# Optimization experiments

Hardware: AMD Instinct MI355X
Metric: run time of the kernel (lower is better)

## Reference

```python
import jax, jax.numpy as jnp
import numpy as np

B, S, D = 2, 2048, 4096
H, KV, HD = 32, 8, 128
THETA = 10000.0


def rotate_half(x):
    x1, x2 = x[..., : HD // 2], x[..., HD // 2 :]
    return jnp.concatenate((-x2, x1), axis=-1)


def setup_inputs() -> dict:
    key = jax.random.key(0)
    ks = jax.random.split(key, 8)
    s = 1.0 / np.sqrt(D)
    return {
        "hidden_states": jax.random.normal(ks[0], (B, S, D), jnp.float32),
        "modality_indicators": jax.random.randint(ks[1], (B, S), 0, 2, jnp.int64 if jax.config.jax_enable_x64 else jnp.int32),
        "position_ids": jnp.arange(S, dtype=jnp.int32),
        "Wq": jax.random.normal(ks[2], (D, H * HD), jnp.float32) * s,
        "Wk0": jax.random.normal(ks[3], (D, KV * HD), jnp.float32) * s,
        "Wk1": jax.random.normal(ks[4], (D, KV * HD), jnp.float32) * s,
        "Wv0": jax.random.normal(ks[5], (D, KV * HD), jnp.float32) * s,
        "Wv1": jax.random.normal(ks[6], (D, KV * HD), jnp.float32) * s,
        "Wo": jax.random.normal(ks[7], (H * HD, D), jnp.float32) * s,
    }


def reference(hidden_states, modality_indicators, position_ids, Wq, Wk0, Wk1, Wv0, Wv1, Wo):
    x = hidden_states
    # Multiway (modality-routed) k/v projections: per-token select between two linears.
    sel = (modality_indicators == 1)[..., None]  # [B,S,1]
    q = x @ Wq                                   # [B,S,H*HD]
    k = jnp.where(sel, x @ Wk1, x @ Wk0)         # [B,S,KV*HD]
    v = jnp.where(sel, x @ Wv1, x @ Wv0)

    q = q.reshape(B, S, H, HD).transpose(0, 2, 1, 3)    # [B,H,S,HD]
    k = k.reshape(B, S, KV, HD).transpose(0, 2, 1, 3)   # [B,KV,S,HD]
    v = v.reshape(B, S, KV, HD).transpose(0, 2, 1, 3)

    # RoPE cache and application (emb = cat(freqs, freqs))
    inv_freq = 1.0 / (THETA ** (jnp.arange(0, HD, 2, dtype=jnp.float32) / HD))
    freqs = position_ids.astype(jnp.float32)[:, None] * inv_freq[None, :]   # [S,HD/2]
    emb = jnp.concatenate((freqs, freqs), axis=-1)                          # [S,HD]
    cos = jnp.cos(emb)[None, None, :, :]                                    # [1,1,S,HD]
    sin = jnp.sin(emb)[None, None, :, :]
    q = q * cos + rotate_half(q) * sin
    k = k * cos + rotate_half(k) * sin

    # GQA: repeat kv heads
    n_rep = H // KV
    k = jnp.repeat(k, n_rep, axis=1)  # [B,H,S,HD]
    v = jnp.repeat(v, n_rep, axis=1)

    scores = jnp.einsum("bhqd,bhkd->bhqk", q, k) / np.sqrt(HD)
    causal = jnp.tril(jnp.ones((S, S), dtype=bool))
    scores = jnp.where(causal[None, None], scores, jnp.finfo(scores.dtype).min)
    attn = jax.nn.softmax(scores, axis=-1)
    ctx = jnp.einsum("bhqk,bhkd->bhqd", attn, v)            # [B,H,S,HD]
    ctx = ctx.transpose(0, 2, 1, 3).reshape(B, S, H * HD)
    return ctx @ Wo
```

## Files before the change

### kernel.cpp

```cpp
#include <hip/hip_runtime.h>

typedef unsigned short u16;
typedef unsigned int   u32;
using bf16x8 = __attribute__((ext_vector_type(8))) __bf16;
using f32x4  = __attribute__((ext_vector_type(4))) float;
using f32x16 = __attribute__((ext_vector_type(16))) float;
using u32x4  = __attribute__((ext_vector_type(4))) unsigned int;


__device__ __forceinline__ u16 f2bf(float f) {
  u32 u = __builtin_bit_cast(u32, f);
  return (u16)((u + 0x7fffu + ((u >> 16) & 1u)) >> 16);
}
__device__ __forceinline__ float bf2f(u16 h) {
  return __builtin_bit_cast(float, (u32)h << 16);
}
__device__ __forceinline__ f32x4 mfma16(bf16x8 a, bf16x8 b, f32x4 c) {
  return __builtin_amdgcn_mfma_f32_16x16x32_bf16(a, b, c, 0, 0, 0);
}
__device__ __forceinline__ f32x16 mfma32(bf16x8 a, bf16x8 b, f32x16 c) {
  return __builtin_amdgcn_mfma_f32_32x32x16_bf16(a, b, c, 0, 0, 0);
}
__device__ __forceinline__ f32x16 zero16() {
  f32x16 z;
#pragma unroll
  for (int i = 0; i < 16; ++i) z[i] = 0.f;
  return z;
}
__device__ __forceinline__ void g2l16(const void* gp, void* lp) {
  __builtin_amdgcn_global_load_lds(
      (__attribute__((address_space(1))) void*)(void*)gp,
      (__attribute__((address_space(3))) void*)lp, 16, 0, 0);
}

__global__ void k_cvt(const float* __restrict__ in, u16* __restrict__ out, int n4) {
  int i = blockIdx.x * 256 + threadIdx.x;
  if (i >= n4) return;
  float4 v = ((const float4*)in)[i];
  ushort4 o;
  o.x = f2bf(v.x); o.y = f2bf(v.y); o.z = f2bf(v.z); o.w = f2bf(v.w);
  ((ushort4*)out)[i] = o;
}

__global__ void k_tcvt(const float* __restrict__ in, u16* __restrict__ out, int K, int N) {
  __shared__ u16 t[32][33];
  int n0 = blockIdx.x * 32, k0 = blockIdx.y * 32;
  int r = threadIdx.x >> 3, c4 = (threadIdx.x & 7) * 4;
  float4 v = *(const float4*)(in + (size_t)(k0 + r) * N + n0 + c4);
  t[c4 + 0][r] = f2bf(v.x);
  t[c4 + 1][r] = f2bf(v.y);
  t[c4 + 2][r] = f2bf(v.z);
  t[c4 + 3][r] = f2bf(v.w);
  __syncthreads();
  ushort4 o;
  o.x = t[r][c4 + 0]; o.y = t[r][c4 + 1]; o.z = t[r][c4 + 2]; o.w = t[r][c4 + 3];
  *(ushort4*)(out + (size_t)(n0 + r) * K + k0 + c4) = o;
}

__global__ void k_scan(const int* __restrict__ mod, int* __restrict__ perm, int* __restrict__ meta) {
  __shared__ int ps[1024];
  const int b = blockIdx.x, t = threadIdx.x;
  perm[b * 2304 + t] = -1;
  perm[b * 2304 + 1024 + t] = -1;
  if (t < 256) perm[b * 2304 + 2048 + t] = -1;
  const int i0 = 2 * t, i1 = 2 * t + 1;
  const int f0 = (mod[b * 2048 + i0] != 1) ? 1 : 0;
  const int f1 = (mod[b * 2048 + i1] != 1) ? 1 : 0;
  const int sum = f0 + f1;
  ps[t] = sum;
  __syncthreads();
  for (int off = 1; off < 1024; off <<= 1) {
    int v = (t >= off) ? ps[t - off] : 0;
    __syncthreads();
    ps[t] += v;
    __syncthreads();
  }
  const int total0 = ps[1023];
  const int excl = ps[t] - sum;
  const int nt0 = (total0 + 255) >> 8;
  const int off1 = nt0 * 256;
  const int s0 = f0 ? excl : off1 + (i0 - excl);
  const int s1 = f1 ? (excl + f0) : off1 + (i1 - (excl + f0));
  perm[b * 2304 + s0] = i0;
  perm[b * 2304 + s1] = i1;
  if (t == 0) { meta[b * 2] = total0; meta[b * 2 + 1] = nt0; }
}

#define TILE_BODY(T, VMLIT, DOSTAGE)                                         \
  {                                                                          \
    asm volatile("s_waitcnt vmcnt(" VMLIT ")" ::: "memory");                 \
    __builtin_amdgcn_s_barrier();                                            \
    __builtin_amdgcn_sched_barrier(0);                                       \
    const u16* base_ = lds + ((T) & 3) * 16384;                              \
    bf16x8 bfr[4], afr[4];                                                   \
    _Pragma("unroll")                                                        \
    for (int nf = 0; nf < 4; ++nf)                                           \
      bfr[nf] = *(const bf16x8*)(base_ + boff + nf * 512);                   \
    _Pragma("unroll")                                                        \
    for (int mf = 0; mf < 4; ++mf)                                           \
      afr[mf] = *(const bf16x8*)(base_ + aoff + mf * 512);                   \
    if (DOSTAGE) stage((T) + 3);                                             \
    __builtin_amdgcn_s_setprio(1);                                           \
    _Pragma("unroll")                                                        \
    for (int mf = 0; mf < 4; ++mf)                                           \
      _Pragma("unroll")                                                      \
      for (int nf = 0; nf < 4; ++nf)                                         \
        acc[mf][nf] = mfma16(afr[mf], bfr[nf], acc[mf][nf]);                 \
    __builtin_amdgcn_s_setprio(0);                                           \
    _Pragma("unroll")                                                        \
    for (int mf = 0; mf < 4; ++mf)                                           \
      afr[mf] = *(const bf16x8*)(base_ + aoff + (mf + 4) * 512);             \
    __builtin_amdgcn_s_setprio(1);                                           \
    _Pragma("unroll")                                                        \
    for (int mf = 0; mf < 4; ++mf)                                           \
      _Pragma("unroll")                                                      \
      for (int nf = 0; nf < 4; ++nf)                                         \
        acc[mf + 4][nf] = mfma16(afr[mf], bfr[nf], acc[mf + 4][nf]);         \
    __builtin_amdgcn_s_setprio(0);                                           \
  }

#define GEMM_MAIN_LOOP()                                                     \
  stage(0); stage(1); stage(2);                                              \
  for (int t = 0; t < 125; ++t) TILE_BODY(t, "8", true);                     \
  TILE_BODY(125, "8", false);                                                \
  TILE_BODY(126, "4", false);                                                \
  TILE_BODY(127, "0", false);

__global__ __launch_bounds__(512, 2) void k_gemm8(const u16* __restrict__ A, const u16* __restrict__ Bt,
                                                  float* __restrict__ Cp) {
  __shared__ u16 lds[4 * 16384];
  const int tid = threadIdx.x, wid = tid >> 6, l = tid & 63, g = l >> 4, li = l & 15;
  const int wr = wid >> 2, wc = wid & 3;
  const int bid = blockIdx.x;
  const int swz = (bid & 7) * 32 + (bid >> 3);
  const int m0 = (swz >> 4) * 256, n0 = (swz & 15) * 256;

  const int bo = wid * 2048 + l * 16;
  const int srow = bo >> 6;
  const int sgg = (l & 3) ^ ((l >> 3) & 3);
  const u16* pA0 = A + (size_t)(m0 + srow) * 4096 + sgg * 8;
  const u16* pA1 = pA0 + (size_t)16 * 4096;
  const u16* pB0 = Bt + (size_t)(n0 + srow) * 4096 + sgg * 8;
  const u16* pB1 = pB0 + (size_t)16 * 4096;

  auto stage = [&](int t) {
    u16* da = (u16*)lds + (t & 3) * 16384 + wid * 1024;
    u16* db = da + 8192;
    g2l16(pA0 + t * 32, da);
    g2l16(pA1 + t * 32, da + 512);
    g2l16(pB0 + t * 32, db);
    g2l16(pB1 + t * 32, db + 512);
  };

  const int lsl8 = (g ^ ((li >> 1) & 3)) * 8;
  const int aoff = (wr * 128 + li) * 32 + lsl8;
  const int boff = 8192 + (wc * 64 + li) * 32 + lsl8;

  const f32x4 vzero = {0.f, 0.f, 0.f, 0.f};
  f32x4 acc[8][4];
#pragma unroll
  for (int m = 0; m < 8; ++m)
#pragma unroll
    for (int n = 0; n < 4; ++n) acc[m][n] = vzero;

  GEMM_MAIN_LOOP();

#pragma unroll
  for (int mf = 0; mf < 8; ++mf)
#pragma unroll
    for (int nf = 0; nf < 4; ++nf)
#pragma unroll
      for (int j = 0; j < 4; ++j) {
        int row = m0 + wr * 128 + mf * 16 + g * 4 + j;
        int col = n0 + wc * 64 + nf * 16 + li;
        Cp[(size_t)row * 4096 + col] = acc[mf][nf][j];
      }
}

__global__ __launch_bounds__(512, 2) void k_gemmQKV(const u16* __restrict__ Xb, const u16* __restrict__ WqT,
                                                    const u16* __restrict__ B0, const u16* __restrict__ B1,
                                                    const int* __restrict__ perm, const int* __restrict__ meta,
                                                    u16* __restrict__ Qr, u16* __restrict__ Ksel,
                                                    u16* __restrict__ Vsel) {
  __shared__ u16 lds[4 * 16384];
  const int tid = threadIdx.x, wid = tid >> 6, l = tid & 63, g = l >> 4, li = l & 15;
  const int wr = wid >> 2, wc = wid & 3;
  const int bid = blockIdx.x;
  const bool isQ = bid < 256;

  const int bo = wid * 2048 + l * 16;
  const int srow = bo >> 6;
  const int sgg = (l & 3) ^ ((l >> 3) & 3);

  int m0 = 0, n0 = 0, bb = 0, tm = 0;
  const u16 *pA0, *pA1, *pB0;
  if (isQ) {
    const int swz = (bid & 7) * 32 + (bid >> 3);
    m0 = (swz >> 4) * 256; n0 = (swz & 15) * 256;
    pA0 = Xb + (size_t)(m0 + srow) * 4096 + sgg * 8;
    pA1 = pA0 + (size_t)16 * 4096;
    pB0 = WqT + (size_t)(n0 + srow) * 4096 + sgg * 8;
  } else {
    const int kb = bid - 256;
    const int seg = kb >> 3;
    n0 = (kb & 7) * 256;
    bb = seg / 9; tm = seg % 9;
    const int nt0 = meta[bb * 2 + 1];
    const u16* Bt = (tm >= nt0) ? B1 : B0;
    int t0 = perm[bb * 2304 + tm * 256 + srow];
    int t1 = perm[bb * 2304 + tm * 256 + srow + 16];
    if (t0 < 0) t0 = 0;
    if (t1 < 0) t1 = 0;
    pA0 = Xb + ((size_t)bb * 2048 + t0) * 4096 + sgg * 8;
    pA1 = Xb + ((size_t)bb * 2048 + t1) * 4096 + sgg * 8;
    pB0 = Bt + (size_t)(n0 + srow) * 4096 + sgg * 8;
  }
  const u16* pB1 = pB0 + (size_t)16 * 4096;

  auto stage = [&](int t) {
    u16* da = (u16*)lds + (t & 3) * 16384 + wid * 1024;
    u16* db = da + 8192;
    g2l16(pA0 + t * 32, da);
    g2l16(pA1 + t * 32, da + 512);
    g2l16(pB0 + t * 32, db);
    g2l16(pB1 + t * 32, db + 512);
  };

  const int lsl8 = (g ^ ((li >> 1) & 3)) * 8;
  const int aoff = (wr * 128 + li) * 32 + lsl8;
  const int boff = 8192 + (wc * 64 + li) * 32 + lsl8;

  const f32x4 vzero = {0.f, 0.f, 0.f, 0.f};
  f32x4 acc[8][4];
#pragma unroll
  for (int m = 0; m < 8; ++m)
#pragma unroll
    for (int n = 0; n < 4; ++n) acc[m][n] = vzero;

  GEMM_MAIN_LOOP();

  if (isQ) {
#pragma unroll
    for (int mf = 0; mf < 8; ++mf)
#pragma unroll
      for (int nf = 0; nf < 4; ++nf)
#pragma unroll
        for (int j = 0; j < 4; ++j) {
          int row = m0 + wr * 128 + mf * 16 + g * 4 + j;
          int col = n0 + wc * 64 + nf * 16 + li;
          int b = row >> 11, s = row & 2047, h = col >> 7, d = col & 127;
          Qr[(((size_t)(b * 32 + h)) * 2048 + s) * 128 + d] = f2bf(acc[mf][nf][j]);
        }
  } else {
#pragma unroll
    for (int mf = 0; mf < 8; ++mf)
#pragma unroll
      for (int nf = 0; nf < 4; ++nf)
#pragma unroll
        for (int j = 0; j < 4; ++j) {
          int slot = tm * 256 + wr * 128 + mf * 16 + g * 4 + j;
          int tok = perm[bb * 2304 + slot];
          if (tok >= 0) {
            int col = n0 + wc * 64 + nf * 16 + li;
            int kv = col >> 10, hh = (col >> 7) & 7, d = col & 127;
            u16* dst = (kv ? Vsel : Ksel) + (((size_t)(bb * 8 + hh)) * 2048 + tok) * 128 + d;
            *dst = f2bf(acc[mf][nf][j]);
          }
        }
  }
}

__global__ void k_ropeq(u16* __restrict__ Q, const int* __restrict__ pos) {
  int row = blockIdx.x * 4 + (threadIdx.x >> 6);
  int l = threadIdx.x & 63;
  int s = row & 2047;
  u16* p = Q + (size_t)row * 128;
  float x1 = bf2f(p[l]), x2 = bf2f(p[l + 64]);
  float ang = (float)pos[s] * expf((float)l * -0.14391156831212787f);
  float cs = cosf(ang), sn = sinf(ang);
  const float sc = 0.08838834764831845f;
  p[l] = f2bf((x1 * cs - x2 * sn) * sc);
  p[l + 64] = f2bf((x2 * cs + x1 * sn) * sc);
}

__global__ void k_kvprep(const u16* __restrict__ Ks, const u16* __restrict__ Vs,
                         const int* __restrict__ pos,
                         u16* __restrict__ Kr, u16* __restrict__ Vt) {
  __shared__ u16 Vl[64][136];
  int blk = blockIdx.x;
  int st = blk & 31, kvh = (blk >> 5) & 7, b = blk >> 8;
  int s0 = st * 64;
  int tid = threadIdx.x, wid = tid >> 6, l = tid & 63;
  float invf = expf((float)l * -0.14391156831212787f);
  size_t slab = (size_t)(b * 8 + kvh) * 2048;
  for (int rr = 0; rr < 16; ++rr) {
    int r = wid * 16 + rr;
    int s = s0 + r;
    const u16* ks = Ks + (slab + s) * 128;
    const u16* vs = Vs + (slab + s) * 128;
    float ang = (float)pos[s] * invf;
    float cs = cosf(ang), sn = sinf(ang);
    float x1 = bf2f(ks[l]), x2 = bf2f(ks[l + 64]);
    u16* kd = Kr + (slab + s) * 128;
    kd[l] = f2bf(x1 * cs - x2 * sn);
    kd[l + 64] = f2bf(x2 * cs + x1 * sn);
    Vl[r][l] = vs[l];
    Vl[r][l + 64] = vs[l + 64];
  }
  __syncthreads();
  int d = tid >> 1, si0 = (tid & 1) * 32;
  u16* vd = Vt + ((size_t)(b * 8 + kvh) * 128 + d) * 2048 + s0 + si0;
#pragma unroll
  for (int k4 = 0; k4 < 8; ++k4) {
    ushort4 o;
    o.x = Vl[si0 + k4 * 4 + 0][d];
    o.y = Vl[si0 + k4 * 4 + 1][d];
    o.z = Vl[si0 + k4 * 4 + 2][d];
    o.w = Vl[si0 + k4 * 4 + 3][d];
    *(ushort4*)(vd + k4 * 4) = o;
  }
}

__global__ __launch_bounds__(256, 2) void k_attn(const u16* __restrict__ Q, const u16* __restrict__ Kr,
                                                 const u16* __restrict__ Vt, u16* __restrict__ ctx) {
  __shared__ u16 Kl[2 * 64 * 128];
  __shared__ u16 Vl[2 * 128 * 64];
  const int bh = blockIdx.x;
  const int p = blockIdx.y;
  const int b = bh >> 5, h = bh & 31, kvh = h >> 2;
  const int tid = threadIdx.x, w = tid >> 6, l = tid & 63;
  const int lo5 = l & 31, hi = l >> 5;
  const bool hib = hi != 0;
  const size_t kvslab = (size_t)(b * 8 + kvh) * 2048;
  const u16* Kg = Kr + kvslab * 128;
  const u16* Vg = Vt + kvslab * 128;
  const float L2E = 1.4426950408889634f;

  auto stage = [&](int kt, int bi) {
#pragma unroll
    for (int i = 0; i < 4; ++i) {
      int c = w * 4 + i;
      int slot = c * 1024 + l * 16;
      {
        int row = slot >> 8;
        int inner = (slot & 255) ^ ((row & 15) << 4);
        g2l16((const char*)Kg + kt * 16384 + row * 256 + inner,
              (char*)Kl + bi * 16384 + c * 1024);
      }
      {
        int row = slot >> 7;
        int inner = (slot & 127) ^ ((row & 7) << 4);
        g2l16((const char*)Vg + (size_t)row * 4096 + kt * 128 + inner,
              (char*)Vl + bi * 16384 + c * 1024);
      }
    }
  };

  for (int hf = 0; hf < 2; ++hf) {
    const int qi = hf ? (15 - p) : p;
    const int q0 = qi * 128;
    const int qlane = q0 + w * 32 + lo5;
    const u16* qrow = Q + ((size_t)bh * 2048 + qlane) * 128;
    bf16x8 qf[8];
#pragma unroll
    for (int kk = 0; kk < 8; ++kk) qf[kk] = *(const bf16x8*)(qrow + kk * 16 + hi * 8);

    f32x16 ot[4];
#pragma unroll
    for (int i = 0; i < 4; ++i) ot[i] = zero16();
    float m = -1e30f, ls = 0.f;

    const int nkt = 2 * qi + 2;
    stage(0, 0);
    stage(1, 1);
    for (int kt = 0; kt < nkt; ++kt) {
      if (kt + 1 < nkt) {
        asm volatile("s_waitcnt vmcnt(8)" ::: "memory");
      } else {
        asm volatile("s_waitcnt vmcnt(0)" ::: "memory");
      }
      __builtin_amdgcn_s_barrier();
      __builtin_amdgcn_sched_barrier(0);
      const char* kbase = (const char*)Kl + (kt & 1) * 16384;
      const char* vbase = (const char*)Vl + (kt & 1) * 16384;
      const int ktb = kt * 64;
      if (ktb <= q0 + w * 32 + 31) {
        f32x16 st[2];
        st[0] = zero16(); st[1] = zero16();
#pragma unroll
        for (int kk = 0; kk < 8; ++kk) {
          bf16x8 kfr[2];
#pragma unroll
          for (int mf = 0; mf < 2; ++mf) {
            int row = mf * 32 + lo5;
            kfr[mf] = *(const bf16x8*)(kbase + row * 256 + ((kk * 32 + hi * 16) ^ ((row & 15) << 4)));
          }
          __builtin_amdgcn_s_setprio(1);
          st[0] = mfma32(kfr[0], qf[kk], st[0]);
          st[1] = mfma32(kfr[1], qf[kk], st[1]);
          __builtin_amdgcn_s_setprio(0);
        }
        if (ktb + 63 > q0 + w * 32) {
#pragma unroll
          for (int mf = 0; mf < 2; ++mf)
#pragma unroll
            for (int r = 0; r < 16; ++r) {
              int kg = ktb + mf * 32 + (r & 3) + 8 * (r >> 2) + 4 * hi;
              if (kg > qlane) st[mf][r] = -3.0e38f;
            }
        }
        float t[16];
#pragma unroll
        for (int r = 0; r < 16; ++r) t[r] = fmaxf(st[0][r], st[1][r]);
#pragma unroll
        for (int s = 8; s >= 1; s >>= 1)
#pragma unroll
          for (int r = 0; r < s; ++r) t[r] = fmaxf(t[r], t[r + s]);
        float pmax = fmaxf(t[0], __shfl_xor(t[0], 32));
        if (!__all(pmax <= m + 8.f)) {
          float nm = fmaxf(m, pmax);
          float resc = exp2f((m - nm) * L2E);
          m = nm;
          ls *= resc;
#pragma unroll
          for (int i = 0; i < 4; ++i)
#pragma unroll
            for (int r = 0; r < 16; ++r) ot[i][r] *= resc;
        }
#pragma unroll
        for (int mf = 0; mf < 2; ++mf)
#pragma unroll
          for (int r = 0; r < 16; ++r) st[mf][r] = exp2f((st[mf][r] - m) * L2E);
        float u[16];
#pragma unroll
        for (int r = 0; r < 16; ++r) u[r] = st[0][r] + st[1][r];
#pragma unroll
        for (int s = 8; s >= 1; s >>= 1)
#pragma unroll
          for (int r = 0; r < s; ++r) u[r] += u[r + s];
        ls += u[0] + __shfl_xor(u[0], 32);
        u32 pkv[16];
#pragma unroll
        for (int mf = 0; mf < 2; ++mf)
#pragma unroll
          for (int tt = 0; tt < 8; ++tt) {
            u32 r;
            asm("v_cvt_pk_bf16_f32 %0, %1, %2" : "=v"(r) : "v"(st[mf][2 * tt]), "v"(st[mf][2 * tt + 1]));
            pkv[mf * 8 + tt] = r;
          }
        bf16x8 pfrag[4];
#pragma unroll
        for (int kk = 0; kk < 4; ++kk) {
          int c = (kk >> 1) * 8 + (kk & 1) * 4;
          u32 m0 = hib ? pkv[c + 2] : pkv[c + 0];
          u32 m1 = hib ? pkv[c + 3] : pkv[c + 1];
          u32 s0 = hib ? pkv[c + 0] : pkv[c + 2];
          u32 s1 = hib ? pkv[c + 1] : pkv[c + 3];
          u32 r0 = (u32)__shfl_xor((int)s0, 32);
          u32 r1 = (u32)__shfl_xor((int)s1, 32);
          u32x4 wv = {hib ? r0 : m0, hib ? r1 : m1, hib ? m0 : r0, hib ? m1 : r1};
          pfrag[kk] = __builtin_bit_cast(bf16x8, wv);
        }
#pragma unroll
        for (int mfV = 0; mfV < 4; ++mfV) {
          int row = mfV * 32 + lo5;
          const char* vb = vbase + row * 128;
          int sw = (row & 7) << 4;
          bf16x8 vf[4];
#pragma unroll
          for (int kk = 0; kk < 4; ++kk)
            vf[kk] = *(const bf16x8*)(vb + ((kk * 32 + hi * 16) ^ sw));
          __builtin_amdgcn_s_setprio(1);
#pragma unroll
          for (int kk = 0; kk < 4; ++kk) ot[mfV] = mfma32(vf[kk], pfrag[kk], ot[mfV]);
          __builtin_amdgcn_s_setprio(0);
        }
      }
      __builtin_amdgcn_s_barrier();
      if (kt + 2 < nkt) stage(kt + 2, kt & 1);
    }
    float inv = 1.0f / ls;
    u16* crow = ctx + ((size_t)(b * 2048) + qlane) * 4096 + h * 128;
#pragma unroll
    for (int mfV = 0; mfV < 4; ++mfV)
#pragma unroll
      for (int rq = 0; rq < 4; ++rq) {
        ushort4 o4;
        o4.x = f2bf(ot[mfV][rq * 4 + 0] * inv);
        o4.y = f2bf(ot[mfV][rq * 4 + 1] * inv);
        o4.z = f2bf(ot[mfV][rq * 4 + 2] * inv);
        o4.w = f2bf(ot[mfV][rq * 4 + 3] * inv);
        *(ushort4*)(crow + mfV * 32 + rq * 8 + hi * 4) = o4;
      }
  }
}

extern "C" void kernel_launch(void* const* d_in, const int* in_sizes, int n_in,
                              void* d_out, int out_size, void* d_ws, size_t ws_size,
                              hipStream_t stream) {
  (void)in_sizes; (void)n_in; (void)out_size; (void)ws_size;
  const float* X   = (const float*)d_in[0];
  const int*   mod = (const int*)d_in[1];
  const int*   pos = (const int*)d_in[2];
  const float* Wq  = (const float*)d_in[3];
  const float* Wk0 = (const float*)d_in[4];
  const float* Wk1 = (const float*)d_in[5];
  const float* Wv0 = (const float*)d_in[6];
  const float* Wv1 = (const float*)d_in[7];
  const float* Wo  = (const float*)d_in[8];
  float* out = (float*)d_out;

  u16* p = (u16*)d_ws;
  auto take = [&](size_t n) { u16* r = p; p += n; return r; };
  u16* Xb    = take(16777216);
  u16* WqT   = take(16777216);
  u16* WoT   = take(16777216);
  u16* Wkv0T = take(8388608);
  u16* Wkv1T = take(8388608);
  u16* Qr    = take(16777216);
  u16* Ksel  = take(4194304);
  u16* Vsel  = take(4194304);
  int* perm  = (int*)take(9216);
  int* meta  = (int*)take(64);
  u16* Kr  = WqT;
  u16* Vtr = WqT + 4194304;
  u16* ctx = Xb;

  k_cvt<<<dim3(16384), 256, 0, stream>>>(X, Xb, 4194304);
  k_scan<<<dim3(2), 1024, 0, stream>>>(mod, perm, meta);
  k_tcvt<<<dim3(128, 128), 256, 0, stream>>>(Wq, WqT, 4096, 4096);
  k_tcvt<<<dim3(32, 128), 256, 0, stream>>>(Wk0, Wkv0T,                4096, 1024);
  k_tcvt<<<dim3(32, 128), 256, 0, stream>>>(Wv0, Wkv0T + 1024 * 4096,  4096, 1024);
  k_tcvt<<<dim3(32, 128), 256, 0, stream>>>(Wk1, Wkv1T,                4096, 1024);
  k_tcvt<<<dim3(32, 128), 256, 0, stream>>>(Wv1, Wkv1T + 1024 * 4096,  4096, 1024);
  k_tcvt<<<dim3(128, 128), 256, 0, stream>>>(Wo, WoT, 4096, 4096);

  k_gemmQKV<<<dim3(400), 512, 0, stream>>>(Xb, WqT, Wkv0T, Wkv1T, perm, meta, Qr, Ksel, Vsel);

  k_ropeq<<<dim3(32768), 256, 0, stream>>>(Qr, pos);
  k_kvprep<<<dim3(512), 256, 0, stream>>>(Ksel, Vsel, pos, Kr, Vtr);

  k_attn<<<dim3(64, 8), 256, 0, stream>>>(Qr, Kr, Vtr, ctx);

  k_gemm8<<<dim3(256), 512, 0, stream>>>(ctx, WoT, out);
}
```

Measured before the change: 570.8 us.

## Split GEMM stage issue across MFMA halves and widen weight transpose tiles

```diff
diff --git a/kernel.cpp b/kernel.cpp
--- a/kernel.cpp
+++ b/kernel.cpp
@@ -6,6 +6,7 @@
 using f32x4  = __attribute__((ext_vector_type(4))) float;
 using f32x16 = __attribute__((ext_vector_type(16))) float;
 using u32x4  = __attribute__((ext_vector_type(4))) unsigned int;
+using ushort8 = __attribute__((ext_vector_type(8))) unsigned short;
 
 
 __device__ __forceinline__ u16 f2bf(float f) {
@@ -42,19 +43,26 @@
   ((ushort4*)out)[i] = o;
 }
 
-__global__ void k_tcvt(const float* __restrict__ in, u16* __restrict__ out, int K, int N) {
-  __shared__ u16 t[32][33];
-  int n0 = blockIdx.x * 32, k0 = blockIdx.y * 32;
-  int r = threadIdx.x >> 3, c4 = (threadIdx.x & 7) * 4;
-  float4 v = *(const float4*)(in + (size_t)(k0 + r) * N + n0 + c4);
-  t[c4 + 0][r] = f2bf(v.x);
-  t[c4 + 1][r] = f2bf(v.y);
-  t[c4 + 2][r] = f2bf(v.z);
-  t[c4 + 3][r] = f2bf(v.w);
+__global__ __launch_bounds__(256) void k_tcvt(const float* __restrict__ in, u16* __restrict__ out,
+                                              int K, int N) {
+  __shared__ u16 t[64][72];
+  const int n0 = blockIdx.x * 64, k0 = blockIdx.y * 64;
+  const int tid = threadIdx.x;
+  const int r = tid >> 2, c4 = (tid & 3) * 16;
+  const float* src = in + (size_t)(k0 + r) * N + n0 + c4;
+#pragma unroll
+  for (int q = 0; q < 4; ++q) {
+    float4 v = *(const float4*)(src + 4 * q);
+    t[c4 + 4 * q + 0][r] = f2bf(v.x);
+    t[c4 + 4 * q + 1][r] = f2bf(v.y);
+    t[c4 + 4 * q + 2][r] = f2bf(v.z);
+    t[c4 + 4 * q + 3][r] = f2bf(v.w);
+  }
   __syncthreads();
-  ushort4 o;
-  o.x = t[r][c4 + 0]; o.y = t[r][c4 + 1]; o.z = t[r][c4 + 2]; o.w = t[r][c4 + 3];
-  *(ushort4*)(out + (size_t)(n0 + r) * K + k0 + c4) = o;
+  u16* dst = out + (size_t)(n0 + r) * K + k0 + c4;
+#pragma unroll
+  for (int hh = 0; hh < 2; ++hh)
+    *(ushort8*)(dst + 8 * hh) = *(const ushort8*)(&t[r][c4 + 8 * hh]);
 }
 
 __global__ void k_scan(const int* __restrict__ mod, int* __restrict__ perm, int* __restrict__ meta) {
@@ -99,7 +107,9 @@
     _Pragma("unroll")                                                        \
     for (int mf = 0; mf < 4; ++mf)                                           \
       afr[mf] = *(const bf16x8*)(base_ + aoff + mf * 512);                   \
-    if (DOSTAGE) stage((T) + 3);                                             \
+    if (DOSTAGE) stageA((T) + 3);                                            \
+    asm volatile("s_waitcnt lgkmcnt(0)" ::: "memory");                       \
+    __builtin_amdgcn_sched_barrier(0);                                       \
     __builtin_amdgcn_s_setprio(1);                                           \
     _Pragma("unroll")                                                        \
     for (int mf = 0; mf < 4; ++mf)                                           \
@@ -107,9 +117,13 @@
       for (int nf = 0; nf < 4; ++nf)                                         \
         acc[mf][nf] = mfma16(afr[mf], bfr[nf], acc[mf][nf]);                 \
     __builtin_amdgcn_s_setprio(0);                                           \
+    __builtin_amdgcn_s_barrier();                                            \
     _Pragma("unroll")                                                        \
     for (int mf = 0; mf < 4; ++mf)                                           \
       afr[mf] = *(const bf16x8*)(base_ + aoff + (mf + 4) * 512);             \
+    if (DOSTAGE) stageB((T) + 3);                                            \
+    asm volatile("s_waitcnt lgkmcnt(0)" ::: "memory");                       \
+    __builtin_amdgcn_sched_barrier(0);                                       \
     __builtin_amdgcn_s_setprio(1);                                           \
     _Pragma("unroll")                                                        \
     for (int mf = 0; mf < 4; ++mf)                                           \
@@ -120,7 +134,7 @@
   }
 
 #define GEMM_MAIN_LOOP()                                                     \
-  stage(0); stage(1); stage(2);                                              \
+  stageA(0); stageB(0); stageA(1); stageB(1); stageA(2); stageB(2);          \
   for (int t = 0; t < 125; ++t) TILE_BODY(t, "8", true);                     \
   TILE_BODY(125, "8", false);                                                \
   TILE_BODY(126, "4", false);                                                \
@@ -143,11 +157,13 @@
   const u16* pB0 = Bt + (size_t)(n0 + srow) * 4096 + sgg * 8;
   const u16* pB1 = pB0 + (size_t)16 * 4096;
 
-  auto stage = [&](int t) {
+  auto stageA = [&](int t) {
     u16* da = (u16*)lds + (t & 3) * 16384 + wid * 1024;
-    u16* db = da + 8192;
     g2l16(pA0 + t * 32, da);
     g2l16(pA1 + t * 32, da + 512);
+  };
+  auto stageB = [&](int t) {
+    u16* db = (u16*)lds + (t & 3) * 16384 + wid * 1024 + 8192;
     g2l16(pB0 + t * 32, db);
     g2l16(pB1 + t * 32, db + 512);
   };
@@ -217,11 +233,13 @@
   }
   const u16* pB1 = pB0 + (size_t)16 * 4096;
 
-  auto stage = [&](int t) {
+  auto stageA = [&](int t) {
     u16* da = (u16*)lds + (t & 3) * 16384 + wid * 1024;
-    u16* db = da + 8192;
     g2l16(pA0 + t * 32, da);
     g2l16(pA1 + t * 32, da + 512);
+  };
+  auto stageB = [&](int t) {
+    u16* db = (u16*)lds + (t & 3) * 16384 + wid * 1024 + 8192;
     g2l16(pB0 + t * 32, db);
     g2l16(pB1 + t * 32, db + 512);
   };
@@ -528,12 +546,12 @@
 
   k_cvt<<<dim3(16384), 256, 0, stream>>>(X, Xb, 4194304);
   k_scan<<<dim3(2), 1024, 0, stream>>>(mod, perm, meta);
-  k_tcvt<<<dim3(128, 128), 256, 0, stream>>>(Wq, WqT, 4096, 4096);
-  k_tcvt<<<dim3(32, 128), 256, 0, stream>>>(Wk0, Wkv0T,                4096, 1024);
-  k_tcvt<<<dim3(32, 128), 256, 0, stream>>>(Wv0, Wkv0T + 1024 * 4096,  4096, 1024);
-  k_tcvt<<<dim3(32, 128), 256, 0, stream>>>(Wk1, Wkv1T,                4096, 1024);
-  k_tcvt<<<dim3(32, 128), 256, 0, stream>>>(Wv1, Wkv1T + 1024 * 4096,  4096, 1024);
-  k_tcvt<<<dim3(128, 128), 256, 0, stream>>>(Wo, WoT, 4096, 4096);
+  k_tcvt<<<dim3(64, 64), 256, 0, stream>>>(Wq, WqT, 4096, 4096);
+  k_tcvt<<<dim3(16, 64), 256, 0, stream>>>(Wk0, Wkv0T,                4096, 1024);
+  k_tcvt<<<dim3(16, 64), 256, 0, stream>>>(Wv0, Wkv0T + 1024 * 4096,  4096, 1024);
+  k_tcvt<<<dim3(16, 64), 256, 0, stream>>>(Wk1, Wkv1T,                4096, 1024);
+  k_tcvt<<<dim3(16, 64), 256, 0, stream>>>(Wv1, Wkv1T + 1024 * 4096,  4096, 1024);
+  k_tcvt<<<dim3(64, 64), 256, 0, stream>>>(Wo, WoT, 4096, 4096);
 
   k_gemmQKV<<<dim3(400), 512, 0, stream>>>(Xb, WqT, Wkv0T, Wkv1T, perm, meta, Qr, Ksel, Vsel);
 
```

Measured after the change: 566.2 us. No clear change (-0.8%).
